# Performance work log

Hardware: AMD Instinct MI355X
Metric: run time of the kernel (lower is better)

Reference implementation:

```python
import jax, jax.numpy as jnp
import numpy as np

EMBED_DIM = 1024
NUM_HEADS = 16
HEAD_DIM = EMBED_DIM // NUM_HEADS


def setup_inputs() -> dict:
    key = jax.random.key(0)
    ks = jax.random.split(key, 9)
    B, S, D = 4, 2048, EMBED_DIM
    s = 1.0 / np.sqrt(D)
    return {
        "x": jax.random.normal(ks[0], (B, S, D), dtype=jnp.float32),
        "Wq": jax.random.normal(ks[1], (D, D), dtype=jnp.float32) * s,
        "bq": jnp.zeros((D,), dtype=jnp.float32),
        "Wk": jax.random.normal(ks[2], (D, D), dtype=jnp.float32) * s,
        "bk": jnp.zeros((D,), dtype=jnp.float32),
        "Wv": jax.random.normal(ks[3], (D, D), dtype=jnp.float32) * s,
        "bv": jnp.zeros((D,), dtype=jnp.float32),
        "Wo": jax.random.normal(ks[4], (D, D), dtype=jnp.float32) * s,
        "bo": jnp.zeros((D,), dtype=jnp.float32),
    }


def reference(x, Wq, bq, Wk, bk, Wv, bv, Wo, bo):
    B, S, D = x.shape
    H, Hd = NUM_HEADS, HEAD_DIM

    def proj(W, b):
        # [B,S,D] -> [B,H,S,Hd]
        y = jnp.einsum('bsd,de->bse', x, W) + b
        return y.reshape(B, S, H, Hd).transpose(0, 2, 1, 3)

    q = proj(Wq, bq)
    k = proj(Wk, bk)
    v = proj(Wv, bv)

    scale = 1.0 / jnp.sqrt(jnp.asarray(Hd, dtype=x.dtype))
    scores = jnp.einsum('bhqd,bhkd->bhqk', q, k) * scale  # [B,H,S,S]
    attn = jax.nn.softmax(scores, axis=-1)
    # dropout is identity in eval/inference mode
    heads = jnp.einsum('bhqk,bhkd->bhqd', attn, v)  # [B,H,S,Hd]
    heads = heads.transpose(0, 2, 1, 3).reshape(B, S, D)
    z = jnp.einsum('bsd,de->bse', heads, Wo) + bo
    return z
```

## Files before the change

kernel.cpp:

```cpp
#include <hip/hip_runtime.h>


typedef __attribute__((ext_vector_type(8))) short bf16x8;
typedef __attribute__((ext_vector_type(4))) float f32x4;

#define MFMA16 __builtin_amdgcn_mfma_f32_16x16x32_bf16

__device__ __forceinline__ unsigned short f2bf(float f) {
  unsigned int u = __float_as_uint(f);
  u += 0x7fff + ((u >> 16) & 1);
  return (unsigned short)(u >> 16);
}

__device__ __forceinline__ void gl2l16(const unsigned short* g, unsigned short* l) {
  __builtin_amdgcn_global_load_lds((const __attribute__((address_space(1))) void*)g,
                                   (__attribute__((address_space(3))) void*)l, 16, 0, 0);
}

__global__ __launch_bounds__(256) void k_convert_x(const float* __restrict__ x,
                                                   unsigned short* __restrict__ xb) {
  int i = (blockIdx.x * 256 + threadIdx.x) * 4;
  float4 v = *(const float4*)(x + i);
  ushort4 u;
  u.x = f2bf(v.x); u.y = f2bf(v.y); u.z = f2bf(v.z); u.w = f2bf(v.w);
  *(ushort4*)(xb + i) = u;
}

__global__ __launch_bounds__(256) void k_transpose_w(const float* w0, const float* w1,
                                                     const float* w2, const float* w3,
                                                     unsigned short* o0, unsigned short* o1,
                                                     unsigned short* o2, unsigned short* o3) {
  const float* W = blockIdx.z == 0 ? w0 : blockIdx.z == 1 ? w1 : blockIdx.z == 2 ? w2 : w3;
  unsigned short* O = blockIdx.z == 0 ? o0 : blockIdx.z == 1 ? o1 : blockIdx.z == 2 ? o2 : o3;
  __shared__ float t[32][33];
  int e0 = blockIdx.x * 32, d0 = blockIdx.y * 32;
  #pragma unroll
  for (int i = 0; i < 4; i++)
    t[threadIdx.y + i * 8][threadIdx.x] = W[(d0 + threadIdx.y + i * 8) * 1024 + e0 + threadIdx.x];
  __syncthreads();
  #pragma unroll
  for (int i = 0; i < 4; i++)
    O[(e0 + threadIdx.y + i * 8) * 1024 + d0 + threadIdx.x] = f2bf(t[threadIdx.x][threadIdx.y + i * 8]);
}

__global__ __launch_bounds__(256) void gemm_qkv(const unsigned short* __restrict__ A,
                                                const unsigned short* __restrict__ BtQ,
                                                const unsigned short* __restrict__ BtK,
                                                const unsigned short* __restrict__ BtV,
                                                const float* __restrict__ biq,
                                                const float* __restrict__ bik,
                                                const float* __restrict__ biv,
                                                unsigned short* __restrict__ oq,
                                                unsigned short* __restrict__ ok,
                                                unsigned short* __restrict__ ov,
                                                float qscale) {
  const int z = blockIdx.z;
  const unsigned short* Bt = z == 0 ? BtQ : z == 1 ? BtK : BtV;
  const float* bias = z == 0 ? biq : z == 1 ? bik : biv;
  unsigned short* out = z == 0 ? oq : z == 1 ? ok : ov;
  const float scale = z == 0 ? qscale : 1.0f;

  const int tid = threadIdx.x;
  const int lane = tid & 63, w = tid >> 6;
  const int wr = (w >> 1) * 64, wc = (w & 1) * 64;
  const int fm = lane & 15, quad = lane >> 4;
  const int bm0 = blockIdx.y * 128, bn0 = blockIdx.x * 128;

  __shared__ unsigned short As[128 * 32];
  __shared__ unsigned short Bs[128 * 32];

  f32x4 acc[4][4] = {};

  const int srow = lane >> 2;
  const int sswz = ((lane & 3) ^ (srow & 3)) * 8;
  const unsigned short* gA = A + (size_t)(bm0 + w * 32 + srow) * 1024 + sswz;
  const unsigned short* gB = Bt + (size_t)(bn0 + w * 32 + srow) * 1024 + sswz;
  unsigned short* lA = As + w * 1024;
  unsigned short* lB = Bs + w * 1024;

  const int cswz = (fm & 3);

  for (int kb = 0; kb < 1024; kb += 32) {
    gl2l16(gA + kb, lA);
    gl2l16(gA + kb + 16 * 1024, lA + 512);
    gl2l16(gB + kb, lB);
    gl2l16(gB + kb + 16 * 1024, lB + 512);
    __syncthreads();
    bf16x8 af[4], bfr[4];
    #pragma unroll
    for (int mt = 0; mt < 4; mt++)
      af[mt] = *(const bf16x8*)&As[(wr + mt * 16 + fm) * 32 + ((quad ^ cswz) * 8)];
    #pragma unroll
    for (int nt = 0; nt < 4; nt++)
      bfr[nt] = *(const bf16x8*)&Bs[(wc + nt * 16 + fm) * 32 + ((quad ^ cswz) * 8)];
    #pragma unroll
    for (int mt = 0; mt < 4; mt++)
      #pragma unroll
      for (int nt = 0; nt < 4; nt++)
        acc[mt][nt] = MFMA16(af[mt], bfr[nt], acc[mt][nt], 0, 0, 0);
    __syncthreads();
  }

  float bv[4];
  #pragma unroll
  for (int nt = 0; nt < 4; nt++) bv[nt] = bias[bn0 + wc + nt * 16 + fm];

  #pragma unroll
  for (int mt = 0; mt < 4; mt++) {
    #pragma unroll
    for (int nt = 0; nt < 4; nt++) {
      #pragma unroll
      for (int r = 0; r < 4; r++) {
        int row = bm0 + wr + mt * 16 + quad * 4 + r;
        int col = bn0 + wc + nt * 16 + fm;
        float v = (acc[mt][nt][r] + bv[nt]) * scale;
        int b = row >> 11, s = row & 2047, h = col >> 6, hd = col & 63;
        if (z < 2)
          out[(((b << 4) + h) * 2048 + s) * 64 + hd] = f2bf(v);
        else
          out[(((b << 4) + h) * 64 + hd) * 2048 + s] = f2bf(v);
      }
    }
  }
}

__global__ __launch_bounds__(256) void gemm_out(const unsigned short* __restrict__ A,
                                                const unsigned short* __restrict__ Bt,
                                                const float* __restrict__ bias,
                                                float* __restrict__ out) {
  const int tid = threadIdx.x;
  const int lane = tid & 63, w = tid >> 6;
  const int wr = (w >> 1) * 64, wc = (w & 1) * 64;
  const int fm = lane & 15, quad = lane >> 4;
  const int bm0 = blockIdx.y * 128, bn0 = blockIdx.x * 128;

  __shared__ unsigned short As[128 * 32];
  __shared__ unsigned short Bs[128 * 32];

  f32x4 acc[4][4] = {};

  const int srow = lane >> 2;
  const int sswz = ((lane & 3) ^ (srow & 3)) * 8;
  const unsigned short* gA = A + (size_t)(bm0 + w * 32 + srow) * 1024 + sswz;
  const unsigned short* gB = Bt + (size_t)(bn0 + w * 32 + srow) * 1024 + sswz;
  unsigned short* lA = As + w * 1024;
  unsigned short* lB = Bs + w * 1024;

  const int cswz = (fm & 3);

  for (int kb = 0; kb < 1024; kb += 32) {
    gl2l16(gA + kb, lA);
    gl2l16(gA + kb + 16 * 1024, lA + 512);
    gl2l16(gB + kb, lB);
    gl2l16(gB + kb + 16 * 1024, lB + 512);
    __syncthreads();
    bf16x8 af[4], bfr[4];
    #pragma unroll
    for (int mt = 0; mt < 4; mt++)
      af[mt] = *(const bf16x8*)&As[(wr + mt * 16 + fm) * 32 + ((quad ^ cswz) * 8)];
    #pragma unroll
    for (int nt = 0; nt < 4; nt++)
      bfr[nt] = *(const bf16x8*)&Bs[(wc + nt * 16 + fm) * 32 + ((quad ^ cswz) * 8)];
    #pragma unroll
    for (int mt = 0; mt < 4; mt++)
      #pragma unroll
      for (int nt = 0; nt < 4; nt++)
        acc[mt][nt] = MFMA16(af[mt], bfr[nt], acc[mt][nt], 0, 0, 0);
    __syncthreads();
  }

  float bv[4];
  #pragma unroll
  for (int nt = 0; nt < 4; nt++) bv[nt] = bias[bn0 + wc + nt * 16 + fm];

  #pragma unroll
  for (int mt = 0; mt < 4; mt++)
    #pragma unroll
    for (int nt = 0; nt < 4; nt++)
      #pragma unroll
      for (int r = 0; r < 4; r++) {
        int row = bm0 + wr + mt * 16 + quad * 4 + r;
        int col = bn0 + wc + nt * 16 + fm;
        out[(size_t)row * 1024 + col] = acc[mt][nt][r] + bv[nt];
      }
}

__global__ __launch_bounds__(256) void k_attn(const unsigned short* __restrict__ q,
                                              const unsigned short* __restrict__ k,
                                              const unsigned short* __restrict__ vt,
                                              unsigned short* __restrict__ heads) {
  const int tid = threadIdx.x, lane = tid & 63, w = tid >> 6;
  const int fm = lane & 15, quad = lane >> 4, k0 = quad * 8;
  const int bh = blockIdx.x, qt = blockIdx.y;
  const int b = bh >> 4, h = bh & 15;
  const unsigned short* qg = q + (size_t)bh * 2048 * 64;
  const unsigned short* kg = k + (size_t)bh * 2048 * 64;
  const unsigned short* vg = vt + (size_t)bh * 64 * 2048;

  __shared__ unsigned short Ks[64 * 64];
  __shared__ unsigned short Vs[64 * 64];
  __shared__ unsigned short Ps[4][16 * 68];

  const int sr = lane >> 3;
  const int sswz = ((lane & 7) ^ sr) * 8;
  const unsigned short* gK = kg + (w * 16 + sr) * 64 + sswz;
  const unsigned short* gV = vg + (size_t)(w * 16 + sr) * 2048 + sswz;
  unsigned short* lK = Ks + w * 1024;
  unsigned short* lV = Vs + w * 1024;

  bf16x8 aq[2][2];
  #pragma unroll
  for (int mt = 0; mt < 2; mt++)
    #pragma unroll
    for (int kh = 0; kh < 2; kh++)
      aq[mt][kh] = *(const bf16x8*)&qg[(qt * 128 + w * 32 + mt * 16 + fm) * 64 + kh * 32 + k0];

  bf16x8 onesf;
  #pragma unroll
  for (int i = 0; i < 8; i++) onesf[i] = (short)0x3F80;

  f32x4 o[2][4] = {};
  f32x4 la[2] = {};
  const int fsw = fm & 7;

  for (int kb = 0; kb < 32; kb++) {
    __syncthreads();
    gl2l16(gK + kb * 4096, lK);
    gl2l16(gK + kb * 4096 + 512, lK + 512);
    gl2l16(gV + kb * 64, lV);
    gl2l16(gV + kb * 64 + 8 * 2048, lV + 512);
    __syncthreads();

    f32x4 s[2][4] = {};
    #pragma unroll
    for (int nt = 0; nt < 4; nt++) {
      #pragma unroll
      for (int kh = 0; kh < 2; kh++) {
        bf16x8 bK = *(const bf16x8*)&Ks[(nt * 16 + fm) * 64 + (((kh * 4 + quad) ^ fsw) * 8)];
        s[0][nt] = MFMA16(aq[0][kh], bK, s[0][nt], 0, 0, 0);
        s[1][nt] = MFMA16(aq[1][kh], bK, s[1][nt], 0, 0, 0);
      }
    }

    bf16x8 ap[2][2];
    #pragma unroll
    for (int mt = 0; mt < 2; mt++) {
      #pragma unroll
      for (int nt = 0; nt < 4; nt++)
        #pragma unroll
        for (int r = 0; r < 4; r++) {
          float p = __builtin_amdgcn_exp2f(s[mt][nt][r]);
          unsigned int t = __float_as_uint(p) + 0x8000u;
          Ps[w][(quad * 4 + r) * 68 + nt * 16 + fm] = (unsigned short)(t >> 16);
        }
      ap[mt][0] = *(const bf16x8*)&Ps[w][fm * 68 + k0];
      ap[mt][1] = *(const bf16x8*)&Ps[w][fm * 68 + 32 + k0];
    }

    #pragma unroll
    for (int ks = 0; ks < 2; ks++) {
      la[0] = MFMA16(ap[0][ks], onesf, la[0], 0, 0, 0);
      la[1] = MFMA16(ap[1][ks], onesf, la[1], 0, 0, 0);
      #pragma unroll
      for (int nt = 0; nt < 4; nt++) {
        bf16x8 bV = *(const bf16x8*)&Vs[(nt * 16 + fm) * 64 + (((ks * 4 + quad) ^ fsw) * 8)];
        o[0][nt] = MFMA16(ap[0][ks], bV, o[0][nt], 0, 0, 0);
        o[1][nt] = MFMA16(ap[1][ks], bV, o[1][nt], 0, 0, 0);
      }
    }
  }

  #pragma unroll
  for (int mt = 0; mt < 2; mt++)
    #pragma unroll
    for (int r = 0; r < 4; r++) {
      float inv = 1.0f / la[mt][r];
      int srw = qt * 128 + w * 32 + mt * 16 + quad * 4 + r;
      #pragma unroll
      for (int nt = 0; nt < 4; nt++)
        heads[(size_t)(b * 2048 + srw) * 1024 + h * 64 + nt * 16 + fm] =
            f2bf(o[mt][nt][r] * inv);
    }
}

extern "C" void kernel_launch(void* const* d_in, const int* in_sizes, int n_in,
                              void* d_out, int out_size, void* d_ws, size_t ws_size,
                              hipStream_t stream) {
  const float* x  = (const float*)d_in[0];
  const float* Wq = (const float*)d_in[1];
  const float* bq = (const float*)d_in[2];
  const float* Wk = (const float*)d_in[3];
  const float* bk = (const float*)d_in[4];
  const float* Wv = (const float*)d_in[5];
  const float* bv = (const float*)d_in[6];
  const float* Wo = (const float*)d_in[7];
  const float* bo = (const float*)d_in[8];
  float* out = (float*)d_out;

  char* ws = (char*)d_ws;
  unsigned short* xb  = (unsigned short*)(ws);
  unsigned short* wtq = (unsigned short*)(ws + (16u << 20));
  unsigned short* wtk = (unsigned short*)(ws + (18u << 20));
  unsigned short* wtv = (unsigned short*)(ws + (20u << 20));
  unsigned short* wto = (unsigned short*)(ws + (22u << 20));
  unsigned short* qb  = (unsigned short*)(ws + (24u << 20));
  unsigned short* kb2 = (unsigned short*)(ws + (40u << 20));
  unsigned short* vtb = (unsigned short*)(ws + (56u << 20));
  unsigned short* hb  = (unsigned short*)(ws + (72u << 20));

  k_convert_x<<<8192, 256, 0, stream>>>(x, xb);
  k_transpose_w<<<dim3(32, 32, 4), dim3(32, 8), 0, stream>>>(Wq, Wk, Wv, Wo, wtq, wtk, wtv, wto);

  const float qscale = 0.125f * 1.44269504088896f;
  gemm_qkv<<<dim3(8, 64, 3), 256, 0, stream>>>(xb, wtq, wtk, wtv, bq, bk, bv,
                                               qb, kb2, vtb, qscale);

  k_attn<<<dim3(64, 16), 256, 0, stream>>>(qb, kb2, vtb, hb);

  gemm_out<<<dim3(8, 64), 256, 0, stream>>>(hb, wto, bo, out);
}
```

Measured before the change: 319.5 us.

## Double GEMM K-tile to 64, merge prep kernels, seed attention MFMA with zero

The two projection GEMMs now stage 64-wide K tiles per iteration through a shared helper, with an 8-way XOR swizzle. This halves the number of barrier pairs per K loop at the cost of twice the LDS per block. The x conversion and weight transpose kernels are merged into one launch, which removes a kernel launch gap. In attention, the first score MFMA takes a zero accumulator directly instead of zero-initialising the score registers.

```diff
diff --git a/kernel.cpp b/kernel.cpp
--- a/kernel.cpp
+++ b/kernel.cpp
@@ -17,30 +17,73 @@
                                    (__attribute__((address_space(3))) void*)l, 16, 0, 0);
 }
 
-__global__ __launch_bounds__(256) void k_convert_x(const float* __restrict__ x,
-                                                   unsigned short* __restrict__ xb) {
-  int i = (blockIdx.x * 256 + threadIdx.x) * 4;
-  float4 v = *(const float4*)(x + i);
-  ushort4 u;
-  u.x = f2bf(v.x); u.y = f2bf(v.y); u.z = f2bf(v.z); u.w = f2bf(v.w);
-  *(ushort4*)(xb + i) = u;
-}
-
-__global__ __launch_bounds__(256) void k_transpose_w(const float* w0, const float* w1,
-                                                     const float* w2, const float* w3,
-                                                     unsigned short* o0, unsigned short* o1,
-                                                     unsigned short* o2, unsigned short* o3) {
-  const float* W = blockIdx.z == 0 ? w0 : blockIdx.z == 1 ? w1 : blockIdx.z == 2 ? w2 : w3;
-  unsigned short* O = blockIdx.z == 0 ? o0 : blockIdx.z == 1 ? o1 : blockIdx.z == 2 ? o2 : o3;
-  __shared__ float t[32][33];
-  int e0 = blockIdx.x * 32, d0 = blockIdx.y * 32;
-  #pragma unroll
-  for (int i = 0; i < 4; i++)
-    t[threadIdx.y + i * 8][threadIdx.x] = W[(d0 + threadIdx.y + i * 8) * 1024 + e0 + threadIdx.x];
-  __syncthreads();
-  #pragma unroll
-  for (int i = 0; i < 4; i++)
-    O[(e0 + threadIdx.y + i * 8) * 1024 + d0 + threadIdx.x] = f2bf(t[threadIdx.x][threadIdx.y + i * 8]);
+__global__ __launch_bounds__(256) void k_prep(const float* __restrict__ x,
+                                              unsigned short* __restrict__ xb,
+                                              const float* w0, const float* w1,
+                                              const float* w2, const float* w3,
+                                              unsigned short* o0, unsigned short* o1,
+                                              unsigned short* o2, unsigned short* o3) {
+  const int bid = blockIdx.x, tid = threadIdx.x;
+  if (bid < 8192) {
+    int i = (bid * 256 + tid) * 4;
+    float4 v = *(const float4*)(x + i);
+    ushort4 u;
+    u.x = f2bf(v.x); u.y = f2bf(v.y); u.z = f2bf(v.z); u.w = f2bf(v.w);
+    *(ushort4*)(xb + i) = u;
+  } else {
+    __shared__ float t[32][33];
+    int tt = bid - 8192;
+    int z = tt >> 10, rem = tt & 1023;
+    const float* W = z == 0 ? w0 : z == 1 ? w1 : z == 2 ? w2 : w3;
+    unsigned short* O = z == 0 ? o0 : z == 1 ? o1 : z == 2 ? o2 : o3;
+    int e0 = (rem & 31) * 32, d0 = (rem >> 5) * 32;
+    int tx = tid & 31, ty = tid >> 5;
+    #pragma unroll
+    for (int i = 0; i < 4; i++)
+      t[ty + i * 8][tx] = W[(d0 + ty + i * 8) * 1024 + e0 + tx];
+    __syncthreads();
+    #pragma unroll
+    for (int i = 0; i < 4; i++)
+      O[(e0 + ty + i * 8) * 1024 + d0 + tx] = f2bf(t[tx][ty + i * 8]);
+  }
+}
+
+__device__ __forceinline__ void kloop64(const unsigned short* __restrict__ gA,
+                                        const unsigned short* __restrict__ gB,
+                                        unsigned short* As, unsigned short* Bs,
+                                        int w, int fm, int quad, int wr, int wc,
+                                        f32x4 (&acc)[4][4]) {
+  const int fsw = fm & 7;
+  const int cs0 = (quad ^ fsw) * 8;
+  const int cs1 = ((quad + 4) ^ fsw) * 8;
+  unsigned short* lA = As + w * 2048;
+  unsigned short* lB = Bs + w * 2048;
+
+  for (int kb = 0; kb < 1024; kb += 64) {
+    __syncthreads();
+    #pragma unroll
+    for (int i = 0; i < 4; i++) {
+      gl2l16(gA + kb + i * 8192, lA + i * 512);
+      gl2l16(gB + kb + i * 8192, lB + i * 512);
+    }
+    __syncthreads();
+    #pragma unroll
+    for (int kh = 0; kh < 2; kh++) {
+      const int cs = kh ? cs1 : cs0;
+      bf16x8 af[4], bfr[4];
+      #pragma unroll
+      for (int mt = 0; mt < 4; mt++)
+        af[mt] = *(const bf16x8*)&As[(wr + mt * 16 + fm) * 64 + cs];
+      #pragma unroll
+      for (int nt = 0; nt < 4; nt++)
+        bfr[nt] = *(const bf16x8*)&Bs[(wc + nt * 16 + fm) * 64 + cs];
+      #pragma unroll
+      for (int mt = 0; mt < 4; mt++)
+        #pragma unroll
+        for (int nt = 0; nt < 4; nt++)
+          acc[mt][nt] = MFMA16(af[mt], bfr[nt], acc[mt][nt], 0, 0, 0);
+    }
+  }
 }
 
 __global__ __launch_bounds__(256) void gemm_qkv(const unsigned short* __restrict__ A,
@@ -66,40 +109,17 @@
   const int fm = lane & 15, quad = lane >> 4;
   const int bm0 = blockIdx.y * 128, bn0 = blockIdx.x * 128;
 
-  __shared__ unsigned short As[128 * 32];
-  __shared__ unsigned short Bs[128 * 32];
+  __shared__ unsigned short As[128 * 64];
+  __shared__ unsigned short Bs[128 * 64];
 
   f32x4 acc[4][4] = {};
 
-  const int srow = lane >> 2;
-  const int sswz = ((lane & 3) ^ (srow & 3)) * 8;
+  const int srow = lane >> 3;
+  const int sswz = ((lane & 7) ^ srow) * 8;
   const unsigned short* gA = A + (size_t)(bm0 + w * 32 + srow) * 1024 + sswz;
   const unsigned short* gB = Bt + (size_t)(bn0 + w * 32 + srow) * 1024 + sswz;
-  unsigned short* lA = As + w * 1024;
-  unsigned short* lB = Bs + w * 1024;
-
-  const int cswz = (fm & 3);
-
-  for (int kb = 0; kb < 1024; kb += 32) {
-    gl2l16(gA + kb, lA);
-    gl2l16(gA + kb + 16 * 1024, lA + 512);
-    gl2l16(gB + kb, lB);
-    gl2l16(gB + kb + 16 * 1024, lB + 512);
-    __syncthreads();
-    bf16x8 af[4], bfr[4];
-    #pragma unroll
-    for (int mt = 0; mt < 4; mt++)
-      af[mt] = *(const bf16x8*)&As[(wr + mt * 16 + fm) * 32 + ((quad ^ cswz) * 8)];
-    #pragma unroll
-    for (int nt = 0; nt < 4; nt++)
-      bfr[nt] = *(const bf16x8*)&Bs[(wc + nt * 16 + fm) * 32 + ((quad ^ cswz) * 8)];
-    #pragma unroll
-    for (int mt = 0; mt < 4; mt++)
-      #pragma unroll
-      for (int nt = 0; nt < 4; nt++)
-        acc[mt][nt] = MFMA16(af[mt], bfr[nt], acc[mt][nt], 0, 0, 0);
-    __syncthreads();
-  }
+
+  kloop64(gA, gB, As, Bs, w, fm, quad, wr, wc, acc);
 
   float bv[4];
   #pragma unroll
@@ -134,40 +154,17 @@
   const int fm = lane & 15, quad = lane >> 4;
   const int bm0 = blockIdx.y * 128, bn0 = blockIdx.x * 128;
 
-  __shared__ unsigned short As[128 * 32];
-  __shared__ unsigned short Bs[128 * 32];
+  __shared__ unsigned short As[128 * 64];
+  __shared__ unsigned short Bs[128 * 64];
 
   f32x4 acc[4][4] = {};
 
-  const int srow = lane >> 2;
-  const int sswz = ((lane & 3) ^ (srow & 3)) * 8;
+  const int srow = lane >> 3;
+  const int sswz = ((lane & 7) ^ srow) * 8;
   const unsigned short* gA = A + (size_t)(bm0 + w * 32 + srow) * 1024 + sswz;
   const unsigned short* gB = Bt + (size_t)(bn0 + w * 32 + srow) * 1024 + sswz;
-  unsigned short* lA = As + w * 1024;
-  unsigned short* lB = Bs + w * 1024;
-
-  const int cswz = (fm & 3);
-
-  for (int kb = 0; kb < 1024; kb += 32) {
-    gl2l16(gA + kb, lA);
-    gl2l16(gA + kb + 16 * 1024, lA + 512);
-    gl2l16(gB + kb, lB);
-    gl2l16(gB + kb + 16 * 1024, lB + 512);
-    __syncthreads();
-    bf16x8 af[4], bfr[4];
-    #pragma unroll
-    for (int mt = 0; mt < 4; mt++)
-      af[mt] = *(const bf16x8*)&As[(wr + mt * 16 + fm) * 32 + ((quad ^ cswz) * 8)];
-    #pragma unroll
-    for (int nt = 0; nt < 4; nt++)
-      bfr[nt] = *(const bf16x8*)&Bs[(wc + nt * 16 + fm) * 32 + ((quad ^ cswz) * 8)];
-    #pragma unroll
-    for (int mt = 0; mt < 4; mt++)
-      #pragma unroll
-      for (int nt = 0; nt < 4; nt++)
-        acc[mt][nt] = MFMA16(af[mt], bfr[nt], acc[mt][nt], 0, 0, 0);
-    __syncthreads();
-  }
+
+  kloop64(gA, gB, As, Bs, w, fm, quad, wr, wc, acc);
 
   float bv[4];
   #pragma unroll
@@ -221,6 +218,7 @@
 
   f32x4 o[2][4] = {};
   f32x4 la[2] = {};
+  const f32x4 zf = {0.f, 0.f, 0.f, 0.f};
   const int fsw = fm & 7;
 
   for (int kb = 0; kb < 32; kb++) {
@@ -231,15 +229,15 @@
     gl2l16(gV + kb * 64 + 8 * 2048, lV + 512);
     __syncthreads();
 
-    f32x4 s[2][4] = {};
+    f32x4 s[2][4];
     #pragma unroll
     for (int nt = 0; nt < 4; nt++) {
-      #pragma unroll
-      for (int kh = 0; kh < 2; kh++) {
-        bf16x8 bK = *(const bf16x8*)&Ks[(nt * 16 + fm) * 64 + (((kh * 4 + quad) ^ fsw) * 8)];
-        s[0][nt] = MFMA16(aq[0][kh], bK, s[0][nt], 0, 0, 0);
-        s[1][nt] = MFMA16(aq[1][kh], bK, s[1][nt], 0, 0, 0);
-      }
+      bf16x8 bK0 = *(const bf16x8*)&Ks[(nt * 16 + fm) * 64 + ((quad ^ fsw) * 8)];
+      s[0][nt] = MFMA16(aq[0][0], bK0, zf, 0, 0, 0);
+      s[1][nt] = MFMA16(aq[1][0], bK0, zf, 0, 0, 0);
+      bf16x8 bK1 = *(const bf16x8*)&Ks[(nt * 16 + fm) * 64 + (((4 + quad) ^ fsw) * 8)];
+      s[0][nt] = MFMA16(aq[0][1], bK1, s[0][nt], 0, 0, 0);
+      s[1][nt] = MFMA16(aq[1][1], bK1, s[1][nt], 0, 0, 0);
     }
 
     bf16x8 ap[2][2];
@@ -308,8 +306,7 @@
   unsigned short* vtb = (unsigned short*)(ws + (56u << 20));
   unsigned short* hb  = (unsigned short*)(ws + (72u << 20));
 
-  k_convert_x<<<8192, 256, 0, stream>>>(x, xb);
-  k_transpose_w<<<dim3(32, 32, 4), dim3(32, 8), 0, stream>>>(Wq, Wk, Wv, Wo, wtq, wtk, wtv, wto);
+  k_prep<<<12288, 256, 0, stream>>>(x, xb, Wq, Wk, Wv, Wo, wtq, wtk, wtv, wto);
 
   const float qscale = 0.125f * 1.44269504088896f;
   gemm_qkv<<<dim3(8, 64, 3), 256, 0, stream>>>(xb, wtq, wtk, wtv, bq, bk, bv,
```

Measured after the change: 302.7 us. 1.06x faster.
